# Optimization experiments

Measured on AMD Instinct MI355X. Metric: run time of the kernel, lower is better.

The kernel has to match this reference:

```python
import jax, jax.numpy as jnp
import numpy as np

B, F, NB, NS, H, W, C, D = 8, 6, 5, 7, 192, 192, 3, 64
LOSS_WEIGHT = 20.0
EPS = 1e-7  # BCE numerical clamp (torch clamps log terms at -100)


def setup_inputs() -> dict:
    key = jax.random.key(0)
    ks = jax.random.split(key, 8)
    return {
        "segmentations": jax.random.uniform(ks[0], (B, F, NB, H, W), jnp.float32),
        "masks": jax.random.uniform(ks[1], (B, F, NS, H, W), jnp.float32),
        "reconstructions": jax.random.normal(ks[2], (B, F, NB, C, H, W), jnp.float32),
        "rec_tgt": jax.random.normal(ks[3], (B, F, C, H, W), jnp.float32),
        "masks_vis": jax.random.uniform(ks[4], (B, F, NS, H, W), jnp.float32),
        "attn_index": jax.random.uniform(ks[5], (B, F, NS, NB), jnp.float32),
        "slots": jax.random.normal(ks[6], (B, F, NS, D), jnp.float32),
        "pred_slots": jax.random.normal(ks[7], (B, F, NS, D), jnp.float32),
    }


def reference(segmentations, masks, reconstructions, rec_tgt, masks_vis,
              attn_index, slots, pred_slots):
    # Loops over buffer(n) x batch(j) x frame(k>=1) x slot(s) collapse to einsums.
    b, f, nb, h, w = segmentations.shape
    ns = masks.shape[2]
    c = rec_tgt.shape[2]

    p = jnp.clip(segmentations[:, 1:], EPS, 1.0 - EPS)      # [b,f-1,nb,h,w]
    t = (masks[:, 1:] > 0.5).astype(p.dtype)                # [b,f-1,ns,h,w]
    vis = (masks_vis[:, 1:] > 0.5).astype(p.dtype)          # [b,f-1,ns,h,w]

    logp = jnp.log(p)
    log1mp = jnp.log1p(-p)
    # BCE(mean over h*w) for every (buffer n, slot s) pair:
    # -mean[t*logp + (1-t)*log(1-p)] = -(einsum(t, logp-log1mp) + sum(log1mp)) / hw
    ce_pos = jnp.einsum('bfnhw,bfshw->bfns', logp - log1mp, t)
    ce_base = jnp.sum(log1mp, axis=(-1, -2))                # [b,f-1,nb]
    bce = -(ce_pos + ce_base[..., None]) / (h * w)          # [b,f-1,nb,ns]

    # masked MSE: sum(vis * (recon - tgt)^2) / C  (vis is 0/1 so vis^2 = vis)
    diff2 = (reconstructions[:, 1:] - rec_tgt[:, 1:, None]) ** 2  # [b,f-1,nb,c,h,w]
    mse = jnp.einsum('bfnchw,bfshw->bfns', diff2, vis) / c

    loss_ns = bce + 0.1 * mse                               # [b,f-1,nb,ns]
    total = jnp.einsum('bfsn,bfns->', attn_index[:, 1:], loss_ns)
    return total / (b * (f - 1) * nb * ns) * LOSS_WEIGHT
```

## Files before the change

### kernel.cpp

```cpp
#include <hip/hip_runtime.h>

#define TPB 64

namespace {
constexpr int B = 8, F = 6, NB = 5, NS = 7, H = 192, W = 192, C = 3;
constexpr int FM1 = F - 1;
constexpr int HW = H * W;
constexpr int HW4 = HW / 4;
constexpr int PAIRS = B * FM1;
constexpr int BPP = HW4 / TPB;
constexpr int NSLOT = 64;
constexpr int SLOT_STRIDE = 16;
constexpr float EPS = 1e-7f;
constexpr float LN2 = 0.69314718055994530942f;
constexpr float K_BCE = LN2 / (float)HW;
constexpr float COEF = 0.1f / (float)C;
}

__device__ __forceinline__ void fma4(float4& acc, float s, const float4& v) {
  acc.x = fmaf(s, v.x, acc.x); acc.y = fmaf(s, v.y, acc.y);
  acc.z = fmaf(s, v.z, acc.z); acc.w = fmaf(s, v.w, acc.w);
}
__device__ __forceinline__ float clampp(float p) {
  return __builtin_amdgcn_fmed3f(p, EPS, 1.0f - EPS);
}
__device__ __forceinline__ float4 step05(float4 v) {
  return make_float4(v.x > 0.5f ? 1.f : 0.f, v.y > 0.5f ? 1.f : 0.f,
                     v.z > 0.5f ? 1.f : 0.f, v.w > 0.5f ? 1.f : 0.f);
}

__global__ __launch_bounds__(TPB, 4) void em_rec_loss_kernel(
    const float* __restrict__ seg,
    const float* __restrict__ masks,
    const float* __restrict__ recon,
    const float* __restrict__ rtgt,
    const float* __restrict__ vis,
    const float* __restrict__ attn,
    float* __restrict__ partial)
{
  const int blk = blockIdx.x;
  const int pair = blk / BPP;
  const int chunk = blk - pair * BPP;
  const int b = pair / FM1;
  const int f = pair - b * FM1 + 1;
  const int bf = b * F + f;

  float aw[NS][NB], av[NS][NB];
  const float* at = attn + (size_t)bf * NS * NB;
  #pragma unroll
  for (int s = 0; s < NS; ++s)
    #pragma unroll
    for (int n = 0; n < NB; ++n) {
      const float a = at[s * NB + n];
      aw[s][n] = a * K_BCE;
      av[s][n] = a * COEF;
    }
  float AK[NB];
  #pragma unroll
  for (int n = 0; n < NB; ++n) {
    float t = 0.f;
    #pragma unroll
    for (int s = 0; s < NS; ++s) t += aw[s][n];
    AK[n] = t;
  }

  const float4* sp = (const float4*)(seg   + (size_t)bf * NB * HW);
  const float4* mp = (const float4*)(masks + (size_t)bf * NS * HW);
  const float4* vp = (const float4*)(vis   + (size_t)bf * NS * HW);
  const float4* rp = (const float4*)(recon + (size_t)bf * NB * C * HW);
  const float4* tp = (const float4*)(rtgt  + (size_t)bf * C * HW);

  const int q = chunk * TPB + threadIdx.x;

  float4 m4[NS], v4[NS];
  #pragma unroll
  for (int s = 0; s < NS; ++s) m4[s] = mp[s * HW4 + q];
  #pragma unroll
  for (int s = 0; s < NS; ++s) v4[s] = vp[s * HW4 + q];
  float4 tg[C];
  #pragma unroll
  for (int c = 0; c < C; ++c) tg[c] = tp[c * HW4 + q];
  float4 p4[NB];
  #pragma unroll
  for (int n = 0; n < NB; ++n) p4[n] = sp[n * HW4 + q];

  float4 wt[NB], wv[NB];
  #pragma unroll
  for (int n = 0; n < NB; ++n) {
    wt[n] = make_float4(0.f, 0.f, 0.f, 0.f);
    wv[n] = make_float4(0.f, 0.f, 0.f, 0.f);
  }
  #pragma unroll
  for (int s = 0; s < NS; ++s) {
    const float4 t4 = step05(m4[s]);
    const float4 vv = step05(v4[s]);
    #pragma unroll
    for (int n = 0; n < NB; ++n) {
      fma4(wt[n], aw[s][n], t4);
      fma4(wv[n], av[s][n], vv);
    }
  }

  float4 acc4 = make_float4(0.f, 0.f, 0.f, 0.f);
  #pragma unroll
  for (int n = 0; n < NB; ++n) {
    float4 p = p4[n];
    p.x = clampp(p.x); p.y = clampp(p.y); p.z = clampp(p.z); p.w = clampp(p.w);
    const float4 g  = make_float4(__log2f(p.x), __log2f(p.y),
                                  __log2f(p.z), __log2f(p.w));
    const float4 g1 = make_float4(__log2f(1.0f - p.x), __log2f(1.0f - p.y),
                                  __log2f(1.0f - p.z), __log2f(1.0f - p.w));
    float4 d2 = make_float4(0.f, 0.f, 0.f, 0.f);
    #pragma unroll
    for (int c = 0; c < C; ++c) {
      const float4 r = rp[(n * C + c) * HW4 + q];
      const float dx = r.x - tg[c].x, dy = r.y - tg[c].y;
      const float dz = r.z - tg[c].z, dw = r.w - tg[c].w;
      d2.x = fmaf(dx, dx, d2.x); d2.y = fmaf(dy, dy, d2.y);
      d2.z = fmaf(dz, dz, d2.z); d2.w = fmaf(dw, dw, d2.w);
    }
    acc4.x = fmaf(g.x, -wt[n].x, fmaf(g1.x, wt[n].x - AK[n], fmaf(d2.x, wv[n].x, acc4.x)));
    acc4.y = fmaf(g.y, -wt[n].y, fmaf(g1.y, wt[n].y - AK[n], fmaf(d2.y, wv[n].y, acc4.y)));
    acc4.z = fmaf(g.z, -wt[n].z, fmaf(g1.z, wt[n].z - AK[n], fmaf(d2.z, wv[n].z, acc4.z)));
    acc4.w = fmaf(g.w, -wt[n].w, fmaf(g1.w, wt[n].w - AK[n], fmaf(d2.w, wv[n].w, acc4.w)));
  }

  float acc = (acc4.x + acc4.y) + (acc4.z + acc4.w);

  #pragma unroll
  for (int off = 32; off > 0; off >>= 1)
    acc += __shfl_down(acc, off, 64);

  if (threadIdx.x == 0) {
    atomicAdd(&partial[(blk & (NSLOT - 1)) * SLOT_STRIDE], acc);
  }
}

__global__ __launch_bounds__(64) void final_reduce(
    const float* __restrict__ partial, float* __restrict__ out)
{
  float v = partial[threadIdx.x * SLOT_STRIDE];
  #pragma unroll
  for (int off = 32; off > 0; off >>= 1)
    v += __shfl_down(v, off, 64);
  if (threadIdx.x == 0) {
    constexpr float SCALE = 20.0f / (float)(B * FM1 * NB * NS);
    out[0] = v * SCALE;
  }
}

extern "C" void kernel_launch(void* const* d_in, const int* in_sizes, int n_in,
                              void* d_out, int out_size, void* d_ws, size_t ws_size,
                              hipStream_t stream) {
  const float* seg   = (const float*)d_in[0];
  const float* masks = (const float*)d_in[1];
  const float* recon = (const float*)d_in[2];
  const float* rtgt  = (const float*)d_in[3];
  const float* vis   = (const float*)d_in[4];
  const float* attn  = (const float*)d_in[5];

  float* out = (float*)d_out;
  float* partial = (float*)d_ws;

  hipMemsetAsync(partial, 0, NSLOT * SLOT_STRIDE * sizeof(float), stream);

  const int grid = PAIRS * BPP;
  em_rec_loss_kernel<<<grid, TPB, 0, stream>>>(seg, masks, recon, rtgt, vis,
                                               attn, partial);
  final_reduce<<<1, 64, 0, stream>>>(partial, out);
}
```

Baseline: 260.2 us.

## Use 256-thread blocks, hoist all loads before compute, fold scales post-reduction

```diff
diff --git a/kernel.cpp b/kernel.cpp
--- a/kernel.cpp
+++ b/kernel.cpp
@@ -1,6 +1,6 @@
 #include <hip/hip_runtime.h>
 
-#define TPB 64
+#define TPB 256
 
 namespace {
 constexpr int B = 8, F = 6, NB = 5, NS = 7, H = 192, W = 192, C = 3;
@@ -29,7 +29,7 @@
                      v.z > 0.5f ? 1.f : 0.f, v.w > 0.5f ? 1.f : 0.f);
 }
 
-__global__ __launch_bounds__(TPB, 4) void em_rec_loss_kernel(
+__global__ __launch_bounds__(TPB, 2) void em_rec_loss_kernel(
     const float* __restrict__ seg,
     const float* __restrict__ masks,
     const float* __restrict__ recon,
@@ -45,25 +45,6 @@
   const int f = pair - b * FM1 + 1;
   const int bf = b * F + f;
 
-  float aw[NS][NB], av[NS][NB];
-  const float* at = attn + (size_t)bf * NS * NB;
-  #pragma unroll
-  for (int s = 0; s < NS; ++s)
-    #pragma unroll
-    for (int n = 0; n < NB; ++n) {
-      const float a = at[s * NB + n];
-      aw[s][n] = a * K_BCE;
-      av[s][n] = a * COEF;
-    }
-  float AK[NB];
-  #pragma unroll
-  for (int n = 0; n < NB; ++n) {
-    float t = 0.f;
-    #pragma unroll
-    for (int s = 0; s < NS; ++s) t += aw[s][n];
-    AK[n] = t;
-  }
-
   const float4* sp = (const float4*)(seg   + (size_t)bf * NB * HW);
   const float4* mp = (const float4*)(masks + (size_t)bf * NS * HW);
   const float4* vp = (const float4*)(vis   + (size_t)bf * NS * HW);
@@ -72,17 +53,36 @@
 
   const int q = chunk * TPB + threadIdx.x;
 
-  float4 m4[NS], v4[NS];
+  float4 m4[NS], v4[NS], tg[C], p4[NB], r4[NB][C];
   #pragma unroll
   for (int s = 0; s < NS; ++s) m4[s] = mp[s * HW4 + q];
   #pragma unroll
   for (int s = 0; s < NS; ++s) v4[s] = vp[s * HW4 + q];
-  float4 tg[C];
   #pragma unroll
   for (int c = 0; c < C; ++c) tg[c] = tp[c * HW4 + q];
-  float4 p4[NB];
   #pragma unroll
   for (int n = 0; n < NB; ++n) p4[n] = sp[n * HW4 + q];
+  #pragma unroll
+  for (int n = 0; n < NB; ++n)
+    #pragma unroll
+    for (int c = 0; c < C; ++c) r4[n][c] = rp[(n * C + c) * HW4 + q];
+
+  float a[NS][NB];
+  const float* at = attn + (size_t)bf * NS * NB;
+  #pragma unroll
+  for (int s = 0; s < NS; ++s)
+    #pragma unroll
+    for (int n = 0; n < NB; ++n) a[s][n] = at[s * NB + n];
+  float A[NB];
+  #pragma unroll
+  for (int n = 0; n < NB; ++n) {
+    float t = 0.f;
+    #pragma unroll
+    for (int s = 0; s < NS; ++s) t += a[s][n];
+    A[n] = t;
+  }
+
+  __builtin_amdgcn_sched_barrier(0);
 
   float4 wt[NB], wv[NB];
   #pragma unroll
@@ -96,12 +96,13 @@
     const float4 vv = step05(v4[s]);
     #pragma unroll
     for (int n = 0; n < NB; ++n) {
-      fma4(wt[n], aw[s][n], t4);
-      fma4(wv[n], av[s][n], vv);
+      fma4(wt[n], a[s][n], t4);
+      fma4(wv[n], a[s][n], vv);
     }
   }
 
-  float4 acc4 = make_float4(0.f, 0.f, 0.f, 0.f);
+  float4 accB = make_float4(0.f, 0.f, 0.f, 0.f);
+  float4 accM = make_float4(0.f, 0.f, 0.f, 0.f);
   #pragma unroll
   for (int n = 0; n < NB; ++n) {
     float4 p = p4[n];
@@ -113,26 +114,39 @@
     float4 d2 = make_float4(0.f, 0.f, 0.f, 0.f);
     #pragma unroll
     for (int c = 0; c < C; ++c) {
-      const float4 r = rp[(n * C + c) * HW4 + q];
-      const float dx = r.x - tg[c].x, dy = r.y - tg[c].y;
-      const float dz = r.z - tg[c].z, dw = r.w - tg[c].w;
+      const float dx = r4[n][c].x - tg[c].x, dy = r4[n][c].y - tg[c].y;
+      const float dz = r4[n][c].z - tg[c].z, dw = r4[n][c].w - tg[c].w;
       d2.x = fmaf(dx, dx, d2.x); d2.y = fmaf(dy, dy, d2.y);
       d2.z = fmaf(dz, dz, d2.z); d2.w = fmaf(dw, dw, d2.w);
     }
-    acc4.x = fmaf(g.x, -wt[n].x, fmaf(g1.x, wt[n].x - AK[n], fmaf(d2.x, wv[n].x, acc4.x)));
-    acc4.y = fmaf(g.y, -wt[n].y, fmaf(g1.y, wt[n].y - AK[n], fmaf(d2.y, wv[n].y, acc4.y)));
-    acc4.z = fmaf(g.z, -wt[n].z, fmaf(g1.z, wt[n].z - AK[n], fmaf(d2.z, wv[n].z, acc4.z)));
-    acc4.w = fmaf(g.w, -wt[n].w, fmaf(g1.w, wt[n].w - AK[n], fmaf(d2.w, wv[n].w, acc4.w)));
+    accB.x = fmaf(g.x, -wt[n].x, fmaf(g1.x, wt[n].x - A[n], accB.x));
+    accB.y = fmaf(g.y, -wt[n].y, fmaf(g1.y, wt[n].y - A[n], accB.y));
+    accB.z = fmaf(g.z, -wt[n].z, fmaf(g1.z, wt[n].z - A[n], accB.z));
+    accB.w = fmaf(g.w, -wt[n].w, fmaf(g1.w, wt[n].w - A[n], accB.w));
+    accM.x = fmaf(d2.x, wv[n].x, accM.x);
+    accM.y = fmaf(d2.y, wv[n].y, accM.y);
+    accM.z = fmaf(d2.z, wv[n].z, accM.z);
+    accM.w = fmaf(d2.w, wv[n].w, accM.w);
   }
 
-  float acc = (acc4.x + acc4.y) + (acc4.z + acc4.w);
+  const float sB = (accB.x + accB.y) + (accB.z + accB.w);
+  const float sM = (accM.x + accM.y) + (accM.z + accM.w);
+  float acc = fmaf(K_BCE, sB, COEF * sM);
 
   #pragma unroll
   for (int off = 32; off > 0; off >>= 1)
     acc += __shfl_down(acc, off, 64);
 
+  __shared__ float wsum[TPB / 64];
+  const int lane = threadIdx.x & 63;
+  const int wid = threadIdx.x >> 6;
+  if (lane == 0) wsum[wid] = acc;
+  __syncthreads();
   if (threadIdx.x == 0) {
-    atomicAdd(&partial[(blk & (NSLOT - 1)) * SLOT_STRIDE], acc);
+    float s = 0.f;
+    #pragma unroll
+    for (int i = 0; i < TPB / 64; ++i) s += wsum[i];
+    atomicAdd(&partial[(blk & (NSLOT - 1)) * SLOT_STRIDE], s);
   }
 }
 
```

Result: no change. 259.2 us (-0.4%).
